# Optimization experiments

Measured on AMD Instinct MI355X. Metric: run time of the kernel, lower is better.

Reference implementation:

```python
import jax, jax.numpy as jnp
import numpy as np

DIM = 1024
NUM_HEADS = 16
HEAD_DIM = DIM // NUM_HEADS
SCALE = HEAD_DIM ** -0.5


def setup_inputs() -> dict:
    key0 = jax.random.key(0)
    ks = jax.random.split(key0, 8)
    B, L, S = 2, 1024, 2048
    inp = {
        "query": jax.random.normal(ks[0], (B, L, DIM), dtype=jnp.float32),
        "key": jax.random.normal(ks[1], (B, S, DIM), dtype=jnp.float32),
        "value": jax.random.normal(ks[2], (B, S, DIM), dtype=jnp.float32),
        # projection weights, stored as [in, out] so x @ W matches torch Linear
        "Wq": jax.random.normal(ks[3], (DIM, DIM), dtype=jnp.float32) * (DIM ** -0.5),
        "Wk": jax.random.normal(ks[4], (DIM, DIM), dtype=jnp.float32) * (DIM ** -0.5),
        "Wv": jax.random.normal(ks[5], (DIM, DIM), dtype=jnp.float32) * (DIM ** -0.5),
        "Wo": jax.random.normal(ks[6], (DIM, DIM), dtype=jnp.float32) * (DIM ** -0.5),
        "bo": jax.random.normal(ks[7], (DIM,), dtype=jnp.float32) * 0.02,
    }
    return inp


def reference(query, key, value, Wq, Wk, Wv, Wo, bo):
    B, L, C = query.shape
    S = key.shape[1]
    H, D = NUM_HEADS, HEAD_DIM
    # QKV projections (no bias), split heads: [B, H, L/S, D]
    q = (query @ Wq).reshape(B, L, H, D).transpose(0, 2, 1, 3)
    k = (key @ Wk).reshape(B, S, H, D).transpose(0, 2, 1, 3)
    v = (value @ Wv).reshape(B, S, H, D).transpose(0, 2, 1, 3)
    # scaled dot-product attention (qk_norm=False -> identity)
    attn = jnp.einsum("bhld,bhsd->bhls", q * SCALE, k)
    attn = jax.nn.softmax(attn, axis=-1)
    x = jnp.einsum("bhls,bhsd->bhld", attn, v)
    x = x.transpose(0, 2, 1, 3).reshape(B, L, C)
    # output projection (with bias)
    return x @ Wo + bo
```

## Files before the change

### kernel.cpp

```cpp
#include <hip/hip_runtime.h>

namespace {

typedef _Float16 f16;
typedef __attribute__((ext_vector_type(2))) _Float16 f16x2;
typedef __attribute__((ext_vector_type(4))) _Float16 f16x4;
typedef __attribute__((ext_vector_type(8))) _Float16 f16x8;
typedef __attribute__((ext_vector_type(4))) float f32x4;
typedef __attribute__((ext_vector_type(16))) float f32x16;

constexpr int kDim   = 1024;
constexpr int kHeads = 16;
constexpr int kHd    = 64;
constexpr int kB     = 2;
constexpr int kL     = 1024;
constexpr int kS     = 2048;

__device__ inline void gload16(const f16* g, f16* l) {
  __builtin_amdgcn_global_load_lds(
      (const __attribute__((address_space(1))) void*)(g),
      (__attribute__((address_space(3))) void*)(l), 16, 0, 0);
}

struct PrepArgs {
  const float* csrc[3];
  f16* cdst[3];
  int cn[3];
  const float* w[4];
  f16* wt[4];
};

__global__ __launch_bounds__(256) void prep(PrepArgs a) {
  __shared__ float T[32][33];
  const int y = blockIdx.y;
  if (y < 3) {
    const int i = (blockIdx.x * 256 + threadIdx.x) * 8;
    if (i >= a.cn[y]) return;
    const float* __restrict__ src = a.csrc[y];
    float4 v0 = *(const float4*)(src + i);
    float4 v1 = *(const float4*)(src + i + 4);
    f16x8 h = {(f16)v0.x, (f16)v0.y, (f16)v0.z, (f16)v0.w,
               (f16)v1.x, (f16)v1.y, (f16)v1.z, (f16)v1.w};
    *(f16x8*)(a.cdst[y] + i) = h;
  } else {
    if (blockIdx.x >= 1024) return;
    const int z = y - 3;
    const float* __restrict__ W = a.w[z];
    f16* __restrict__ Wt = a.wt[z];
    const int n0 = (blockIdx.x & 31) * 32;
    const int k0 = (blockIdx.x >> 5) * 32;
    const int r = threadIdx.x >> 3;
    const int c = (threadIdx.x & 7) * 4;
    float4 v = *(const float4*)(W + (size_t)(k0 + r) * kDim + n0 + c);
    T[c + 0][r] = v.x; T[c + 1][r] = v.y; T[c + 2][r] = v.z; T[c + 3][r] = v.w;
    __syncthreads();
    f16x4 h = {(f16)T[r][c], (f16)T[r][c + 1], (f16)T[r][c + 2], (f16)T[r][c + 3]};
    *(f16x4*)(Wt + (size_t)(n0 + r) * kDim + k0 + c) = h;
  }
}

struct ProjArgs {
  const f16* A[3];
  const f16* Bt[3];
  f16* C[3];
};

__global__ __launch_bounds__(256) void gemm_proj(ProjArgs p) {
  constexpr int K = kDim;
  constexpr int NI = K / 32;
  int bx = (blockIdx.x & 7) * 80 + (blockIdx.x >> 3);
  int z, m0, n0, Nz;
  if (bx < 128)      { z = 0; m0 = (bx >> 3) * 128; n0 = (bx & 7) * 128; Nz = kDim; }
  else if (bx < 384) { bx -= 128; z = 1; m0 = (bx >> 3) * 128; n0 = (bx & 7) * 128; Nz = kDim; }
  else               { bx -= 384; z = 2; m0 = (bx >> 5) * 128; n0 = (bx & 31) * 128; Nz = kB * kS; }
  const f16* __restrict__ A  = p.A[z];
  const f16* __restrict__ Bt = p.Bt[z];
  f16* __restrict__ C = p.C[z];

  __shared__ __align__(16) f16 As[2][128 * 32];
  __shared__ __align__(16) f16 Bs[2][128 * 32];
  const int t = threadIdx.x;
  const int lane = t & 63;
  const int wave = t >> 6;
  const int wm = (wave >> 1) * 64;
  const int wn = (wave & 1) * 64;
  const int col = lane & 15;
  const int quad = lane >> 4;

  f32x4 acc[4][4];
#pragma unroll
  for (int i = 0; i < 4; ++i)
#pragma unroll
    for (int j = 0; j < 4; ++j) acc[i][j] = (f32x4){0.f, 0.f, 0.f, 0.f};

  const int c0 = t, c1 = t + 256;
  const f16* a0 = A + (size_t)(m0 + (c0 >> 2)) * K + (c0 & 3) * 8;
  const f16* a1 = A + (size_t)(m0 + (c1 >> 2)) * K + (c1 & 3) * 8;
  const f16* b0 = Bt + (size_t)(n0 + (c0 >> 2)) * K + (c0 & 3) * 8;
  const f16* b1 = Bt + (size_t)(n0 + (c1 >> 2)) * K + (c1 & 3) * 8;
  f16* const as0 = As[0] + c0 * 8;
  f16* const as1 = As[0] + c1 * 8;
  f16* const bs0 = Bs[0] + c0 * 8;
  f16* const bs1 = Bs[0] + c1 * 8;
  constexpr int kBuf = 128 * 32;

  gload16(a0, as0);
  gload16(a1, as1);
  gload16(b0, bs0);
  gload16(b1, bs1);
  __syncthreads();

  for (int i = 0; i < NI; ++i) {
    const int cur = i & 1;
    if (i + 1 < NI) {
      const int ko = (i + 1) * 32;
      const int nb = (1 - cur) * kBuf;
      gload16(a0 + ko, as0 + nb);
      gload16(a1 + ko, as1 + nb);
      gload16(b0 + ko, bs0 + nb);
      gload16(b1 + ko, bs1 + nb);
    }

    f16x8 af[4], bf[4];
#pragma unroll
    for (int mt = 0; mt < 4; ++mt)
      af[mt] = *(const f16x8*)(As[cur] + (wm + mt * 16 + col) * 32 + quad * 8);
#pragma unroll
    for (int nt = 0; nt < 4; ++nt)
      bf[nt] = *(const f16x8*)(Bs[cur] + (wn + nt * 16 + col) * 32 + quad * 8);
#pragma unroll
    for (int mt = 0; mt < 4; ++mt)
#pragma unroll
      for (int nt = 0; nt < 4; ++nt)
        acc[mt][nt] = __builtin_amdgcn_mfma_f32_16x16x32_f16(
            af[mt], bf[nt], acc[mt][nt], 0, 0, 0);

    __syncthreads();
  }

  const int crow = m0 + wm + quad * 4;
  const int ccol = n0 + wn + col;
#pragma unroll
  for (int mt = 0; mt < 4; ++mt)
#pragma unroll
    for (int nt = 0; nt < 4; ++nt)
#pragma unroll
      for (int r = 0; r < 4; ++r)
        C[(size_t)(crow + mt * 16 + r) * Nz + ccol + nt * 16] =
            (f16)acc[mt][nt][r];
}

__global__ __launch_bounds__(256) void gemm_out(
    const f16* __restrict__ A, const f16* __restrict__ Bt,
    const float* __restrict__ bias, float* __restrict__ C, int M, int N, int K)
{
  __shared__ __align__(16) f16 As[2][64 * 32];
  __shared__ __align__(16) f16 Bs[2][64 * 32];
  const int t = threadIdx.x;
  const int lane = t & 63;
  const int wave = t >> 6;
  const int swz = (blockIdx.x & 7) * 64 + (blockIdx.x >> 3);
  const int n0 = (swz & 15) * 64;
  const int m0 = (swz >> 4) * 64;
  const int wm = (wave >> 1) * 32;
  const int wn = (wave & 1) * 32;
  const int col = lane & 15;
  const int quad = lane >> 4;
  const int NI = K / 32;
  constexpr int kBuf = 64 * 32;

  f32x4 acc[2][2];
#pragma unroll
  for (int i = 0; i < 2; ++i)
#pragma unroll
    for (int j = 0; j < 2; ++j) acc[i][j] = (f32x4){0.f, 0.f, 0.f, 0.f};

  const f16* a0 = A + (size_t)(m0 + (t >> 2)) * K + (t & 3) * 8;
  const f16* b0 = Bt + (size_t)(n0 + (t >> 2)) * K + (t & 3) * 8;
  f16* const as0 = As[0] + t * 8;
  f16* const bs0 = Bs[0] + t * 8;

  gload16(a0, as0);
  gload16(b0, bs0);
  __syncthreads();

  for (int i = 0; i < NI; ++i) {
    const int cur = i & 1;
    if (i + 1 < NI) {
      const int ko = (i + 1) * 32;
      const int nb = (1 - cur) * kBuf;
      gload16(a0 + ko, as0 + nb);
      gload16(b0 + ko, bs0 + nb);
    }

    f16x8 af[2], bf[2];
#pragma unroll
    for (int mt = 0; mt < 2; ++mt)
      af[mt] = *(const f16x8*)(As[cur] + (wm + mt * 16 + col) * 32 + quad * 8);
#pragma unroll
    for (int nt = 0; nt < 2; ++nt)
      bf[nt] = *(const f16x8*)(Bs[cur] + (wn + nt * 16 + col) * 32 + quad * 8);
#pragma unroll
    for (int mt = 0; mt < 2; ++mt)
#pragma unroll
      for (int nt = 0; nt < 2; ++nt)
        acc[mt][nt] = __builtin_amdgcn_mfma_f32_16x16x32_f16(
            af[mt], bf[nt], acc[mt][nt], 0, 0, 0);

    __syncthreads();
  }

  const int crow = m0 + wm + quad * 4;
  const int ccol = n0 + wn + col;
#pragma unroll
  for (int mt = 0; mt < 2; ++mt)
#pragma unroll
    for (int nt = 0; nt < 2; ++nt) {
      const float bv = bias[ccol + nt * 16];
#pragma unroll
      for (int r = 0; r < 4; ++r)
        C[(size_t)(crow + mt * 16 + r) * N + ccol + nt * 16] =
            acc[mt][nt][r] + bv;
    }
}


__device__ inline unsigned pk2f(float a, float b) {
  union { f16x2 h; unsigned u; } c;
  c.h = f16x2{(f16)a, (f16)b};
  return c.u;
}

__device__ inline void swap32(unsigned& x, unsigned& y) {
  asm("v_permlane32_swap_b32 %0, %1" : "+v"(x), "+v"(y));
}

__global__ __launch_bounds__(256, 2) void flash_attn_mfma4(
    const f16* __restrict__ q, const f16* __restrict__ k,
    const f16* __restrict__ vT, f16* __restrict__ x)
{
  constexpr int LP  = 72;
  constexpr int NT2 = (kS / 2) / 64;
  __shared__ __align__(16) f16 Kt[2][2][64 * LP];
  __shared__ __align__(16) f16 Vt[2][2][64 * LP];

  const int t    = threadIdx.x;
  const int lane = t & 63;
  const int wave = t >> 6;
  const int wq   = wave & 1;
  const int wh   = wave >> 1;
  const int ln   = lane & 31;
  const int hi   = lane >> 5;
  const int bh   = blockIdx.x;
  const int l0   = blockIdx.y * 64;
  const int h    = bh & (kHeads - 1);
  const int b    = bh >> 4;

  f16x8 qf[4];
  {
    const f16* src = q + ((size_t)b * kL + l0 + wq * 32 + ln) * kDim + h * kHd + hi * 8;
#pragma unroll
    for (int ks = 0; ks < 4; ++ks) {
      qf[ks] = *(const f16x8*)(src + ks * 16);
#pragma unroll
      for (int u = 0; u < 8; ++u) qf[ks][u] *= (f16)0.125f;
    }
  }

  const int srow = t >> 2;
  const int scol = (t & 3) * 16;
  const f16* kb = k + ((size_t)b * kS + srow) * kDim + h * kHd + scol;
  const f16* vb = vT + ((size_t)(h * kHd + srow)) * (kB * kS) + b * kS + scol;
  const size_t kHalf = (size_t)1024 * kDim;

  f32x16 accO[2];
#pragma unroll
  for (int dt = 0; dt < 2; ++dt)
#pragma unroll
    for (int r = 0; r < 16; ++r) accO[dt][r] = 0.f;
  float lsum = 0.f;

  f16x8 kh0a, kh0b, kh1a, kh1b, vh0a, vh0b, vh1a, vh1b;

#define STAGE_LOAD(i)                                                   \
  { const f16* kp0 = kb + (size_t)(i) * 64 * kDim;                      \
    const f16* kp1 = kp0 + kHalf;                                       \
    const f16* vp0 = vb + (i) * 64;                                     \
    const f16* vp1 = vp0 + 1024;                                        \
    kh0a = *(const f16x8*)(kp0); kh0b = *(const f16x8*)(kp0 + 8);       \
    kh1a = *(const f16x8*)(kp1); kh1b = *(const f16x8*)(kp1 + 8);       \
    vh0a = *(const f16x8*)(vp0); vh0b = *(const f16x8*)(vp0 + 8);       \
    vh1a = *(const f16x8*)(vp1); vh1b = *(const f16x8*)(vp1 + 8); }

#define STAGE_WRITE(bf)                                                 \
  { f16* kd0 = &Kt[bf][0][srow * LP + scol];                            \
    f16* kd1 = &Kt[bf][1][srow * LP + scol];                            \
    f16* vd0 = &Vt[bf][0][srow * LP + scol];                            \
    f16* vd1 = &Vt[bf][1][srow * LP + scol];                            \
    *(f16x8*)(kd0) = kh0a; *(f16x8*)(kd0 + 8) = kh0b;                   \
    *(f16x8*)(kd1) = kh1a; *(f16x8*)(kd1 + 8) = kh1b;                   \
    *(f16x8*)(vd0) = vh0a; *(f16x8*)(vd0 + 8) = vh0b;                   \
    *(f16x8*)(vd1) = vh1a; *(f16x8*)(vd1 + 8) = vh1b; }

  STAGE_LOAD(0);
  STAGE_WRITE(0);

  for (int i = 0; i < NT2; ++i) {
    const int cur = i & 1;
    if (i + 1 < NT2) STAGE_LOAD(i + 1);
    __syncthreads();

    const f16* Kc = &Kt[cur][wh][0];
    const f16* Vc = &Vt[cur][wh][0];

    f16x8 pf[4];
#pragma unroll
    for (int sub = 0; sub < 2; ++sub) {
      f32x16 s;
#pragma unroll
      for (int r = 0; r < 16; ++r) s[r] = 0.f;
      __builtin_amdgcn_s_setprio(1);
#pragma unroll
      for (int ks = 0; ks < 4; ++ks) {
        f16x8 kf = *(const f16x8*)(Kc + (sub * 32 + ln) * LP + ks * 16 + hi * 8);
        s = __builtin_amdgcn_mfma_f32_32x32x16_f16(kf, qf[ks], s, 0, 0, 0);
      }
      __builtin_amdgcn_s_setprio(0);

      float pp[16];
#pragma unroll
      for (int r = 0; r < 16; ++r) { pp[r] = __expf(s[r]); lsum += pp[r]; }

#pragma unroll
      for (int kk = 0; kk < 2; ++kk) {
        unsigned a0 = pk2f(pp[8 * kk + 0], pp[8 * kk + 1]);
        unsigned a1 = pk2f(pp[8 * kk + 2], pp[8 * kk + 3]);
        unsigned b0 = pk2f(pp[8 * kk + 4], pp[8 * kk + 5]);
        unsigned b1 = pk2f(pp[8 * kk + 6], pp[8 * kk + 7]);
        swap32(a0, b0);
        swap32(a1, b1);
        union { unsigned u[4]; f16x8 v; } w;
        w.u[0] = a0; w.u[1] = a1; w.u[2] = b0; w.u[3] = b1;
        pf[sub * 2 + kk] = w.v;
      }
    }

    __builtin_amdgcn_s_setprio(1);
#pragma unroll
    for (int dt = 0; dt < 2; ++dt)
#pragma unroll
      for (int ks = 0; ks < 4; ++ks) {
        f16x8 vf = *(const f16x8*)(Vc + (dt * 32 + ln) * LP + ks * 16 + hi * 8);
        accO[dt] = __builtin_amdgcn_mfma_f32_32x32x16_f16(pf[ks], vf, accO[dt], 0, 0, 0);
      }
    __builtin_amdgcn_s_setprio(0);

    if (i + 1 < NT2) STAGE_WRITE(1 - cur);
  }
#undef STAGE_LOAD
#undef STAGE_WRITE

  lsum += __shfl_xor(lsum, 32);
  __syncthreads();
  float* sc = (float*)&Kt[0][0][0];
  float* sl = sc + 128 * 33;
  if (wh == 1) {
    float* dst = sc + (wq * 64 + lane) * 33;
#pragma unroll
    for (int dt = 0; dt < 2; ++dt)
#pragma unroll
      for (int r = 0; r < 16; ++r) dst[dt * 16 + r] = accO[dt][r];
    sl[wq * 64 + lane] = lsum;
  }
  __syncthreads();
  if (wh == 0) {
    const float* src = sc + (wq * 64 + lane) * 33;
#pragma unroll
    for (int dt = 0; dt < 2; ++dt)
#pragma unroll
      for (int r = 0; r < 16; ++r) accO[dt][r] += src[dt * 16 + r];
    const float inv = 1.f / (lsum + sl[wq * 64 + lane]);
    const size_t row0 = (size_t)b * kL + l0 + wq * 32;
    f16* xb = x + row0 * kDim + h * kHd + ln;
#pragma unroll
    for (int r = 0; r < 16; ++r) {
      const int qr = (r & 3) + 8 * (r >> 2) + 4 * hi;
      const float invr = __shfl(inv, qr);
      xb[(size_t)qr * kDim]      = (f16)(accO[0][r] * invr);
      xb[(size_t)qr * kDim + 32] = (f16)(accO[1][r] * invr);
    }
  }
}

}

extern "C" void kernel_launch(void* const* d_in, const int* in_sizes, int n_in,
                              void* d_out, int out_size, void* d_ws, size_t ws_size,
                              hipStream_t stream) {
  const float* query = (const float*)d_in[0];
  const float* key   = (const float*)d_in[1];
  const float* value = (const float*)d_in[2];
  const float* Wq    = (const float*)d_in[3];
  const float* Wk    = (const float*)d_in[4];
  const float* Wv    = (const float*)d_in[5];
  const float* Wo    = (const float*)d_in[6];
  const float* bo    = (const float*)d_in[7];
  float* out = (float*)d_out;

  f16* ws = (f16*)d_ws;
  f16* qh  = ws;
  f16* kh  = qh + (size_t)kB * kL * kDim;
  f16* vh  = kh + (size_t)kB * kS * kDim;
  f16* wqt = vh + (size_t)kB * kS * kDim;
  f16* wkt = wqt + (size_t)kDim * kDim;
  f16* wvt = wkt + (size_t)kDim * kDim;
  f16* wot = wvt + (size_t)kDim * kDim;
  f16* qp  = wot + (size_t)kDim * kDim;
  f16* kp  = qp + (size_t)kB * kL * kDim;
  f16* vpT = kp + (size_t)kB * kS * kDim;
  f16* xh  = vpT + (size_t)kB * kS * kDim;

  PrepArgs pr;
  pr.csrc[0] = query; pr.cdst[0] = qh; pr.cn[0] = kB * kL * kDim;
  pr.csrc[1] = key;   pr.cdst[1] = kh; pr.cn[1] = kB * kS * kDim;
  pr.csrc[2] = value; pr.cdst[2] = vh; pr.cn[2] = kB * kS * kDim;
  pr.w[0] = Wq; pr.wt[0] = wqt;
  pr.w[1] = Wk; pr.wt[1] = wkt;
  pr.w[2] = Wv; pr.wt[2] = wvt;
  pr.w[3] = Wo; pr.wt[3] = wot;
  prep<<<dim3(2048, 7), 256, 0, stream>>>(pr);

  ProjArgs pa;
  pa.A[0] = qh;  pa.Bt[0] = wqt; pa.C[0] = qp;
  pa.A[1] = kh;  pa.Bt[1] = wkt; pa.C[1] = kp;
  pa.A[2] = wvt; pa.Bt[2] = vh;  pa.C[2] = vpT;
  gemm_proj<<<dim3(640), 256, 0, stream>>>(pa);

  flash_attn_mfma4<<<dim3(kB * kHeads, kL / 64), 256, 0, stream>>>(
      qp, kp, vpT, xh);

  gemm_out<<<dim3(512), 256, 0, stream>>>(
      xh, wot, bo, out, kB * kL, kDim, kDim);
}
```

Before: 180.6 us.

## Replace async LDS loads in output GEMM with register-staged double buffering

The output projection GEMM now fetches each next K-slice into registers with ordinary global loads and writes it to the other shared-memory buffer after the MFMAs, instead of using direct global-to-LDS loads. It also drops the block-index swizzle in favour of a plain 2D grid. In the attention kernel the barrier moves ahead of the next-stage prefetch. The intent is to overlap global loads with compute using a simpler pipeline, at the cost of more registers and the L2 locality the swizzle provided.

After: 179.8 us. About the same (-0.5%).

```diff
diff --git a/kernel.cpp b/kernel.cpp
--- a/kernel.cpp
+++ b/kernel.cpp
@@ -159,15 +159,13 @@
   const int t = threadIdx.x;
   const int lane = t & 63;
   const int wave = t >> 6;
-  const int swz = (blockIdx.x & 7) * 64 + (blockIdx.x >> 3);
-  const int n0 = (swz & 15) * 64;
-  const int m0 = (swz >> 4) * 64;
+  const int n0 = blockIdx.x * 64;
+  const int m0 = blockIdx.y * 64;
   const int wm = (wave >> 1) * 32;
   const int wn = (wave & 1) * 32;
   const int col = lane & 15;
   const int quad = lane >> 4;
   const int NI = K / 32;
-  constexpr int kBuf = 64 * 32;
 
   f32x4 acc[2][2];
 #pragma unroll
@@ -177,20 +175,23 @@
 
   const f16* a0 = A + (size_t)(m0 + (t >> 2)) * K + (t & 3) * 8;
   const f16* b0 = Bt + (size_t)(n0 + (t >> 2)) * K + (t & 3) * 8;
-  f16* const as0 = As[0] + t * 8;
-  f16* const bs0 = Bs[0] + t * 8;
-
-  gload16(a0, as0);
-  gload16(b0, bs0);
-  __syncthreads();
+
+  {
+    f16x8 ra0 = *(const f16x8*)(a0);
+    f16x8 rb0 = *(const f16x8*)(b0);
+    *(f16x8*)(As[0] + t * 8) = ra0;
+    *(f16x8*)(Bs[0] + t * 8) = rb0;
+  }
 
   for (int i = 0; i < NI; ++i) {
     const int cur = i & 1;
+    __syncthreads();
+
+    f16x8 na0, nb0;
     if (i + 1 < NI) {
       const int ko = (i + 1) * 32;
-      const int nb = (1 - cur) * kBuf;
-      gload16(a0 + ko, as0 + nb);
-      gload16(b0 + ko, bs0 + nb);
+      na0 = *(const f16x8*)(a0 + ko);
+      nb0 = *(const f16x8*)(b0 + ko);
     }
 
     f16x8 af[2], bf[2];
@@ -207,7 +208,11 @@
         acc[mt][nt] = __builtin_amdgcn_mfma_f32_16x16x32_f16(
             af[mt], bf[nt], acc[mt][nt], 0, 0, 0);
 
-    __syncthreads();
+    if (i + 1 < NI) {
+      const int nxt = 1 - cur;
+      *(f16x8*)(As[nxt] + t * 8) = na0;
+      *(f16x8*)(Bs[nxt] + t * 8) = nb0;
+    }
   }
 
   const int crow = m0 + wm + quad * 4;
@@ -307,8 +312,8 @@
 
   for (int i = 0; i < NT2; ++i) {
     const int cur = i & 1;
+    __syncthreads();
     if (i + 1 < NT2) STAGE_LOAD(i + 1);
-    __syncthreads();
 
     const f16* Kc = &Kt[cur][wh][0];
     const f16* Vc = &Vt[cur][wh][0];
@@ -439,6 +444,6 @@
   flash_attn_mfma4<<<dim3(kB * kHeads, kL / 64), 256, 0, stream>>>(
       qp, kp, vpT, xh);
 
-  gemm_out<<<dim3(512), 256, 0, stream>>>(
+  gemm_out<<<dim3(kDim / 64, (kB * kL) / 64), 256, 0, stream>>>(
       xh, wot, bo, out, kB * kL, kDim, kDim);
 }
```
